# Performance work log

Hardware: AMD Instinct MI355X
Metric: run time of the kernel (lower is better)

Reference implementation:

```python
import jax, jax.numpy as jnp
import numpy as np

EMBED_DIM = 128
B, N = 8, 2048


def entmax15(z):
    """Exact 1.5-entmax along the last axis (Peters & Martins 2019, sort-based)."""
    z = z / 2.0
    z = z - jnp.max(z, axis=-1, keepdims=True)  # shift-invariance -> numerical stability
    zs = -jnp.sort(-z, axis=-1)                 # descending sort
    n = z.shape[-1]
    k = jnp.arange(1, n + 1, dtype=z.dtype)
    mean = jnp.cumsum(zs, axis=-1) / k
    meansq = jnp.cumsum(zs * zs, axis=-1) / k
    ss = k * (meansq - mean * mean)
    delta = (1.0 - ss) / k
    delta_safe = jnp.where(delta > 0, delta, 1.0)
    tau = mean - jnp.where(delta > 0, jnp.sqrt(delta_safe), 0.0)
    support = jnp.sum((tau <= zs).astype(jnp.int32), axis=-1, keepdims=True)
    tau_star = jnp.take_along_axis(tau, support - 1, axis=-1)
    return jnp.square(jnp.maximum(z - tau_star, 0.0))


def setup_inputs() -> dict:
    key = jax.random.key(0)
    ks = jax.random.split(key, 6)
    s = 1.0 / np.sqrt(EMBED_DIM)  # torch nn.Linear default init range
    return {
        "x_c": jax.random.normal(ks[0], (B, N, EMBED_DIM), jnp.float32),
        "x_n": jax.random.normal(ks[1], (B, N, EMBED_DIM), jnp.float32),
        "Wq": jax.random.uniform(ks[2], (EMBED_DIM, EMBED_DIM), jnp.float32, -s, s),
        "bq": jax.random.uniform(ks[3], (EMBED_DIM,), jnp.float32, -s, s),
        "Wk": jax.random.uniform(ks[4], (EMBED_DIM, EMBED_DIM), jnp.float32, -s, s),
        "bk": jax.random.uniform(ks[5], (EMBED_DIM,), jnp.float32, -s, s),
    }


def reference(x_c, x_n, Wq, bq, Wk, bk):
    Q = x_c @ Wq.T + bq                      # [B,N,D]
    K = x_n @ Wk.T + bk                      # [B,N,D]
    A = jnp.einsum("bnd,bmd->bnm", Q, K) / jnp.sqrt(jnp.float32(EMBED_DIM))
    # entmax15 sparse normalization over keys; dropout is identity in eval mode
    return entmax15(A)
```

## Files before the change

kernel.cpp:

```cpp
#include <hip/hip_runtime.h>
#include <hip/hip_bf16.h>

#define BATCH 8
#define SEQ   2048
#define DIM   128
#define NROWS 16384
#define THETA_SPAN 22.62741699796952f

typedef __bf16    bf16x8   __attribute__((ext_vector_type(8)));
typedef float     floatx4  __attribute__((ext_vector_type(4)));
typedef _Float16  half2v   __attribute__((ext_vector_type(2)));

static __device__ __forceinline__ unsigned short f2bf(float v) {
    union { __hip_bfloat16 h; unsigned short u; } c;
    c.h = __float2bfloat16(v);
    return c.u;
}
static __device__ __forceinline__ float bf2f(unsigned short u) {
    union { unsigned int i; float f; } c;
    c.i = (unsigned int)u << 16;
    return c.f;
}
static __device__ __forceinline__ unsigned short f2h(float v) {
    union { _Float16 h; unsigned short u; } c;
    c.h = (_Float16)v;
    return c.u;
}

#if __has_builtin(__builtin_amdgcn_fdot2)
static __device__ __forceinline__ float fdot2acc(half2v a, half2v b, float c) {
    return __builtin_amdgcn_fdot2(a, b, c, false);
}
#else
static __device__ __forceinline__ float fdot2acc(half2v a, half2v b, float c) {
    return fmaf((float)a.y, (float)b.y, fmaf((float)a.x, (float)b.x, c));
}
#endif

__global__ void __launch_bounds__(256)
proj_qk(const float* __restrict__ xq, const float* __restrict__ xn,
        const float* __restrict__ Wq, const float* __restrict__ bq,
        const float* __restrict__ Wk, const float* __restrict__ bk,
        unsigned short* __restrict__ Qhi, unsigned short* __restrict__ Qlo,
        unsigned short* __restrict__ Kb) {
    const int isK = blockIdx.y;
    const float* __restrict__ X    = isK ? xn : xq;
    const float* __restrict__ W    = isK ? Wk : Wq;
    const float* __restrict__ bias = isK ? bk : bq;

    __shared__ float wt[64][133];
    __shared__ float xs[64][68];
    const int tid  = threadIdx.x;
    const int l    = tid & 15;
    const int kthi = tid >> 4;
    const int row0 = blockIdx.x * 64;

    float s[4][8];
#pragma unroll
    for (int rr = 0; rr < 4; ++rr)
#pragma unroll
        for (int j = 0; j < 8; ++j) s[rr][j] = 0.0f;

    for (int ph = 0; ph < 2; ++ph) {
        const int e0 = ph * 64;
#pragma unroll
        for (int i = 0; i < 8; ++i) {
            const int g  = tid + 256 * i;
            const int d  = g >> 4;
            const int c4 = g & 15;
            float4 wv = *reinterpret_cast<const float4*>(
                W + (size_t)d * DIM + e0 + 4 * c4);
            wt[4*c4+0][d] = wv.x;  wt[4*c4+1][d] = wv.y;
            wt[4*c4+2][d] = wv.z;  wt[4*c4+3][d] = wv.w;
        }
#pragma unroll
        for (int i = 0; i < 4; ++i) {
            const int g  = tid + 256 * i;
            const int r  = g >> 4;
            const int c4 = g & 15;
            float4 xv = *reinterpret_cast<const float4*>(
                X + (size_t)(row0 + r) * DIM + e0 + 4 * c4);
            *reinterpret_cast<float4*>(&xs[r][4 * c4]) = xv;
        }
        __syncthreads();
#pragma unroll 8
        for (int e = 0; e < 64; ++e) {
            float w8[8];
            *reinterpret_cast<float4*>(w8)     =
                *reinterpret_cast<const float4*>(&wt[e][kthi * 8]);
            *reinterpret_cast<float4*>(w8 + 4) =
                *reinterpret_cast<const float4*>(&wt[e][kthi * 8 + 4]);
#pragma unroll
            for (int rr = 0; rr < 4; ++rr) {
                const float xv = xs[l + 16 * rr][e];
#pragma unroll
                for (int j = 0; j < 8; ++j) s[rr][j] = fmaf(xv, w8[j], s[rr][j]);
            }
        }
        __syncthreads();
    }

    float b8[8];
    *reinterpret_cast<float4*>(b8)     = *reinterpret_cast<const float4*>(bias + kthi * 8);
    *reinterpret_cast<float4*>(b8 + 4) = *reinterpret_cast<const float4*>(bias + kthi * 8 + 4);

    if (!isK) {
#pragma unroll
        for (int rr = 0; rr < 4; ++rr) {
            const int row = row0 + l + 16 * rr;
            union { uint4 v; unsigned short u[8]; } ph_, pl_;
#pragma unroll
            for (int j = 0; j < 8; ++j) {
                const float v = s[rr][j] + b8[j];
                const unsigned short h = f2bf(v);
                ph_.u[j] = h;
                pl_.u[j] = f2bf(v - bf2f(h));
            }
            const size_t base = ((size_t)kthi * NROWS + row) * 8;
            *reinterpret_cast<uint4*>(Qhi + base) = ph_.v;
            *reinterpret_cast<uint4*>(Qlo + base) = pl_.v;
        }
    } else {
#pragma unroll
        for (int rr = 0; rr < 4; ++rr) {
            const int row = row0 + l + 16 * rr;
            const int b   = row >> 11;
            const int key = row & (SEQ - 1);
            union { uint4 v; unsigned short u[8]; } pk;
#pragma unroll
            for (int j = 0; j < 8; ++j) pk.u[j] = f2bf(s[rr][j] + b8[j]);
            const size_t base = (((size_t)(b * 16) + kthi) * SEQ + key) * 8;
            *reinterpret_cast<uint4*>(Kb + base) = pk.v;
        }
    }
}

__global__ void __launch_bounds__(512, 4)
attn_fused(const __bf16* __restrict__ Qhi, const __bf16* __restrict__ Qlo,
           const __bf16* __restrict__ Kb, float* __restrict__ out) {
    __shared__ unsigned int SW[4 * 4098];
    const int tid  = threadIdx.x;
    const int wv   = tid >> 6;
    const int lane = tid & 63;
    const int l4   = lane & 15;
    const int quad = lane >> 4;
    const int row0 = blockIdx.x * 16;
    const int b    = row0 >> 11;
    const int key0 = wv * 256;

    {
        floatx4 acc[16];
        const floatx4 zerov = {};
#pragma unroll
        for (int t = 0; t < 16; ++t) acc[t] = zerov;

        const size_t qbase = ((size_t)quad * NROWS + row0 + l4) * 8;
        const size_t kbase = (((size_t)(b * 16) + quad) * SEQ + key0 + l4) * 8;
        const size_t qstep = (size_t)4 * NROWS * 8;
        const size_t kstep = (size_t)4 * SEQ * 8;

#pragma unroll
        for (int kt = 0; kt < 4; ++kt) {
            const bf16x8 ah = *reinterpret_cast<const bf16x8*>(Qhi + qbase + kt * qstep);
            const bf16x8 al = *reinterpret_cast<const bf16x8*>(Qlo + qbase + kt * qstep);
            const __bf16* kc = Kb + kbase + kt * kstep;
#pragma unroll
            for (int t = 0; t < 16; ++t) {
                const bf16x8 bkv = *reinterpret_cast<const bf16x8*>(kc + (size_t)t * 128);
                acc[t] = __builtin_amdgcn_mfma_f32_16x16x32_bf16(ah, bkv, acc[t], 0, 0, 0);
                acc[t] = __builtin_amdgcn_mfma_f32_16x16x32_bf16(al, bkv, acc[t], 0, 0, 0);
            }
        }
#pragma unroll
        for (int t = 0; t < 16; ++t) {
            union { uint2 v; unsigned short u[4]; } pk;
#pragma unroll
            for (int bb = 0; bb < 4; ++bb) pk.u[bb] = f2h(acc[t][bb]);
            const int key = key0 + t * 16 + l4;
            *reinterpret_cast<uint2*>(&SW[quad * 4098 + 2 * key]) = pk.v;
        }
    }
    __syncthreads();

    const int g  = wv >> 1;
    const int sp = wv & 1;

    const unsigned int* Sw = &SW[g * 4098];
    unsigned int raw[32];
#pragma unroll
    for (int c = 0; c < 32; ++c) raw[c] = Sw[2 * (c * 64 + lane) + sp];

    half2v z0[16], z1[16];
#pragma unroll
    for (int i = 0; i < 16; ++i) {
        union { unsigned int u; half2v h; } c0, c1;
        c0.u = __builtin_amdgcn_perm(raw[2 * i + 1], raw[2 * i], 0x05040100u);
        c1.u = __builtin_amdgcn_perm(raw[2 * i + 1], raw[2 * i], 0x07060302u);
        z0[i] = c0.h;
        z1[i] = c1.h;
    }

    const half2v hzero = {(_Float16)0.0f, (_Float16)0.0f};

    float m0 = -1e30f, m1 = -1e30f;
#pragma unroll
    for (int i = 0; i < 16; ++i) {
        m0 = fmaxf(m0, fmaxf((float)z0[i].x, (float)z0[i].y));
        m1 = fmaxf(m1, fmaxf((float)z1[i].x, (float)z1[i].y));
    }
#pragma unroll
    for (int off = 32; off >= 1; off >>= 1) {
        m0 = fmaxf(m0, __shfl_xor(m0, off, 64));
        m1 = fmaxf(m1, __shfl_xor(m1, off, 64));
    }

    float lo0 = m0 - THETA_SPAN, hi0 = m0;
    float lo1 = m1 - THETA_SPAN, hi1 = m1;
    for (int it = 0; it < 11; ++it) {
        const float th0 = 0.5f * (lo0 + hi0);
        const float th1 = 0.5f * (lo1 + hi1);
        const _Float16 t0h = (_Float16)th0;
        const _Float16 t1h = (_Float16)th1;
        const half2v n0 = {(_Float16)-t0h, (_Float16)-t0h};
        const half2v n1 = {(_Float16)-t1h, (_Float16)-t1h};
        float f0 = 0.0f, f1 = 0.0f;
#pragma unroll
        for (int i = 0; i < 16; ++i) {
            half2v d0 = z0[i] + n0;
            half2v d1 = z1[i] + n1;
            d0 = __builtin_elementwise_max(d0, hzero);
            d1 = __builtin_elementwise_max(d1, hzero);
            f0 = fdot2acc(d0, d0, f0);
            f1 = fdot2acc(d1, d1, f1);
        }
#pragma unroll
        for (int off = 32; off >= 1; off >>= 1) {
            f0 += __shfl_xor(f0, off, 64);
            f1 += __shfl_xor(f1, off, 64);
        }
        if (f0 >= 512.0f) lo0 = th0; else hi0 = th0;
        if (f1 >= 512.0f) lo1 = th1; else hi1 = th1;
    }
    float th0 = 0.5f * (lo0 + hi0);
    float th1 = 0.5f * (lo1 + hi1);
    th0 = (float)((_Float16)th0);
    th1 = (float)((_Float16)th1);

    float* o0 = out + (size_t)(row0 + 4 * g + 2 * sp + 0) * SEQ + lane;
    float* o1 = out + (size_t)(row0 + 4 * g + 2 * sp + 1) * SEQ + lane;
#pragma unroll
    for (int i = 0; i < 16; ++i) {
        const float a0 = fmaxf((float)z0[i].x - th0, 0.0f);
        const float a1 = fmaxf((float)z0[i].y - th0, 0.0f);
        const float b0 = fmaxf((float)z1[i].x - th1, 0.0f);
        const float b1 = fmaxf((float)z1[i].y - th1, 0.0f);
        o0[(size_t)(2 * i) * 64]     = a0 * a0 * (1.0f / 512.0f);
        o0[(size_t)(2 * i + 1) * 64] = a1 * a1 * (1.0f / 512.0f);
        o1[(size_t)(2 * i) * 64]     = b0 * b0 * (1.0f / 512.0f);
        o1[(size_t)(2 * i + 1) * 64] = b1 * b1 * (1.0f / 512.0f);
    }
}

extern "C" void kernel_launch(void* const* d_in, const int* in_sizes, int n_in,
                              void* d_out, int out_size, void* d_ws, size_t ws_size,
                              hipStream_t stream) {
    const float* x_c = (const float*)d_in[0];
    const float* x_n = (const float*)d_in[1];
    const float* Wq  = (const float*)d_in[2];
    const float* bq  = (const float*)d_in[3];
    const float* Wk  = (const float*)d_in[4];
    const float* bk  = (const float*)d_in[5];
    float* out = (float*)d_out;

    char* ws = (char*)d_ws;
    unsigned short* Qhi = (unsigned short*)ws;
    unsigned short* Qlo = (unsigned short*)(ws + ((size_t)4 << 20));
    unsigned short* Kbl = (unsigned short*)(ws + ((size_t)8 << 20));

    proj_qk<<<dim3(NROWS / 64, 2), 256, 0, stream>>>(
        x_c, x_n, Wq, bq, Wk, bk, Qhi, Qlo, Kbl);
    attn_fused<<<NROWS / 16, 512, 0, stream>>>(
        (const __bf16*)Qhi, (const __bf16*)Qlo, (const __bf16*)Kbl, out);
}
```

Measured before the change: 200.7 us.

## Compute Q/K projections with bf16 MFMA using split-precision inputs

Replaces the scalar FP32 FMA projection with MFMA 16x16x32 bf16 instructions. X is split into hi/lo bf16 parts and W is rounded to bf16. Results are staged in shared memory and then written out in the same packed layouts. This moves the small projection GEMM onto matrix cores. W now uses a single bf16 term, so the projection loses some precision, which could shift entmax support near the threshold.

Result: faster. 193.6 us (-3.5%).

```diff
diff --git a/kernel.cpp b/kernel.cpp
--- a/kernel.cpp
+++ b/kernel.cpp
@@ -37,7 +37,7 @@
 }
 #endif
 
-__global__ void __launch_bounds__(256)
+__global__ void __launch_bounds__(256, 2)
 proj_qk(const float* __restrict__ xq, const float* __restrict__ xn,
         const float* __restrict__ Wq, const float* __restrict__ bq,
         const float* __restrict__ Wk, const float* __restrict__ bk,
@@ -48,89 +48,114 @@
     const float* __restrict__ W    = isK ? Wk : Wq;
     const float* __restrict__ bias = isK ? bk : bq;
 
-    __shared__ float wt[64][133];
-    __shared__ float xs[64][68];
+    __shared__ __align__(16) unsigned short SM[34816];
+    unsigned short* XH = SM;
+    unsigned short* XL = SM + 8704;
+    unsigned short* WW = SM + 17408;
+
     const int tid  = threadIdx.x;
+    const int lane = tid & 63;
+    const int wv   = tid >> 6;
+    const int l4   = lane & 15;
+    const int quad = lane >> 4;
+    const int row0 = blockIdx.x * 64;
+
+#pragma unroll
+    for (int i = 0; i < 8; ++i) {
+        const int g  = tid + 256 * i;
+        const int r  = g >> 5;
+        const int c4 = g & 31;
+        const float4 xv = *reinterpret_cast<const float4*>(
+            X + (size_t)(row0 + r) * DIM + 4 * c4);
+        union { ushort2 v[2]; unsigned short u[4]; } hh, ll;
+        const float xf[4] = {xv.x, xv.y, xv.z, xv.w};
+#pragma unroll
+        for (int j = 0; j < 4; ++j) {
+            const unsigned short h = f2bf(xf[j]);
+            hh.u[j] = h;
+            ll.u[j] = f2bf(xf[j] - bf2f(h));
+        }
+        *reinterpret_cast<uint2*>(&XH[r * 136 + 4 * c4]) =
+            *reinterpret_cast<uint2*>(hh.u);
+        *reinterpret_cast<uint2*>(&XL[r * 136 + 4 * c4]) =
+            *reinterpret_cast<uint2*>(ll.u);
+    }
+#pragma unroll
+    for (int i = 0; i < 16; ++i) {
+        const int g  = tid + 256 * i;
+        const int d  = g >> 5;
+        const int c4 = g & 31;
+        const float4 wvv = *reinterpret_cast<const float4*>(
+            W + (size_t)d * DIM + 4 * c4);
+        union { uint2 v; unsigned short u[4]; } pw;
+        pw.u[0] = f2bf(wvv.x); pw.u[1] = f2bf(wvv.y);
+        pw.u[2] = f2bf(wvv.z); pw.u[3] = f2bf(wvv.w);
+        *reinterpret_cast<uint2*>(&WW[d * 136 + 4 * c4]) = pw.v;
+    }
+    __syncthreads();
+
+    floatx4 acc[8];
+    const floatx4 zerov = {};
+#pragma unroll
+    for (int mt = 0; mt < 8; ++mt) acc[mt] = zerov;
+
+#pragma unroll
+    for (int kt = 0; kt < 4; ++kt) {
+        const int koff = kt * 32 + quad * 8;
+        const bf16x8 xh = *reinterpret_cast<const bf16x8*>(
+            &XH[(wv * 16 + l4) * 136 + koff]);
+        const bf16x8 xl = *reinterpret_cast<const bf16x8*>(
+            &XL[(wv * 16 + l4) * 136 + koff]);
+#pragma unroll
+        for (int mt = 0; mt < 8; ++mt) {
+            const bf16x8 wf = *reinterpret_cast<const bf16x8*>(
+                &WW[(mt * 16 + l4) * 136 + koff]);
+            acc[mt] = __builtin_amdgcn_mfma_f32_16x16x32_bf16(wf, xh, acc[mt], 0, 0, 0);
+            acc[mt] = __builtin_amdgcn_mfma_f32_16x16x32_bf16(wf, xl, acc[mt], 0, 0, 0);
+        }
+    }
+
+    const int erow = wv * 16 + l4;
+#pragma unroll
+    for (int mt = 0; mt < 8; ++mt) {
+        const float4 bv = *reinterpret_cast<const float4*>(bias + mt * 16 + quad * 4);
+        const float bf[4] = {bv.x, bv.y, bv.z, bv.w};
+        union { uint2 v; unsigned short u[4]; } hh, ll;
+#pragma unroll
+        for (int r = 0; r < 4; ++r) {
+            const float v = acc[mt][r] + bf[r];
+            const unsigned short h = f2bf(v);
+            hh.u[r] = h;
+            ll.u[r] = f2bf(v - bf2f(h));
+        }
+        const int off = erow * 136 + mt * 16 + quad * 4;
+        *reinterpret_cast<uint2*>(&XH[off]) = hh.v;
+        if (!isK) *reinterpret_cast<uint2*>(&XL[off]) = ll.v;
+    }
+    __syncthreads();
+
     const int l    = tid & 15;
     const int kthi = tid >> 4;
-    const int row0 = blockIdx.x * 64;
-
-    float s[4][8];
-#pragma unroll
-    for (int rr = 0; rr < 4; ++rr)
-#pragma unroll
-        for (int j = 0; j < 8; ++j) s[rr][j] = 0.0f;
-
-    for (int ph = 0; ph < 2; ++ph) {
-        const int e0 = ph * 64;
-#pragma unroll
-        for (int i = 0; i < 8; ++i) {
-            const int g  = tid + 256 * i;
-            const int d  = g >> 4;
-            const int c4 = g & 15;
-            float4 wv = *reinterpret_cast<const float4*>(
-                W + (size_t)d * DIM + e0 + 4 * c4);
-            wt[4*c4+0][d] = wv.x;  wt[4*c4+1][d] = wv.y;
-            wt[4*c4+2][d] = wv.z;  wt[4*c4+3][d] = wv.w;
-        }
-#pragma unroll
-        for (int i = 0; i < 4; ++i) {
-            const int g  = tid + 256 * i;
-            const int r  = g >> 4;
-            const int c4 = g & 15;
-            float4 xv = *reinterpret_cast<const float4*>(
-                X + (size_t)(row0 + r) * DIM + e0 + 4 * c4);
-            *reinterpret_cast<float4*>(&xs[r][4 * c4]) = xv;
-        }
-        __syncthreads();
-#pragma unroll 8
-        for (int e = 0; e < 64; ++e) {
-            float w8[8];
-            *reinterpret_cast<float4*>(w8)     =
-                *reinterpret_cast<const float4*>(&wt[e][kthi * 8]);
-            *reinterpret_cast<float4*>(w8 + 4) =
-                *reinterpret_cast<const float4*>(&wt[e][kthi * 8 + 4]);
-#pragma unroll
-            for (int rr = 0; rr < 4; ++rr) {
-                const float xv = xs[l + 16 * rr][e];
-#pragma unroll
-                for (int j = 0; j < 8; ++j) s[rr][j] = fmaf(xv, w8[j], s[rr][j]);
-            }
-        }
-        __syncthreads();
-    }
-
-    float b8[8];
-    *reinterpret_cast<float4*>(b8)     = *reinterpret_cast<const float4*>(bias + kthi * 8);
-    *reinterpret_cast<float4*>(b8 + 4) = *reinterpret_cast<const float4*>(bias + kthi * 8 + 4);
-
     if (!isK) {
 #pragma unroll
         for (int rr = 0; rr < 4; ++rr) {
-            const int row = row0 + l + 16 * rr;
-            union { uint4 v; unsigned short u[8]; } ph_, pl_;
-#pragma unroll
-            for (int j = 0; j < 8; ++j) {
-                const float v = s[rr][j] + b8[j];
-                const unsigned short h = f2bf(v);
-                ph_.u[j] = h;
-                pl_.u[j] = f2bf(v - bf2f(h));
-            }
-            const size_t base = ((size_t)kthi * NROWS + row) * 8;
-            *reinterpret_cast<uint4*>(Qhi + base) = ph_.v;
-            *reinterpret_cast<uint4*>(Qlo + base) = pl_.v;
+            const int row = l + 16 * rr;
+            const uint4 ph = *reinterpret_cast<const uint4*>(&XH[row * 136 + kthi * 8]);
+            const uint4 pl = *reinterpret_cast<const uint4*>(&XL[row * 136 + kthi * 8]);
+            const size_t base = ((size_t)kthi * NROWS + row0 + row) * 8;
+            *reinterpret_cast<uint4*>(Qhi + base) = ph;
+            *reinterpret_cast<uint4*>(Qlo + base) = pl;
         }
     } else {
 #pragma unroll
         for (int rr = 0; rr < 4; ++rr) {
-            const int row = row0 + l + 16 * rr;
-            const int b   = row >> 11;
-            const int key = row & (SEQ - 1);
-            union { uint4 v; unsigned short u[8]; } pk;
-#pragma unroll
-            for (int j = 0; j < 8; ++j) pk.u[j] = f2bf(s[rr][j] + b8[j]);
+            const int row = l + 16 * rr;
+            const int grow = row0 + row;
+            const int b    = grow >> 11;
+            const int key  = grow & (SEQ - 1);
+            const uint4 pk = *reinterpret_cast<const uint4*>(&XH[row * 136 + kthi * 8]);
             const size_t base = (((size_t)(b * 16) + kthi) * SEQ + key) * 8;
-            *reinterpret_cast<uint4*>(Kb + base) = pk.v;
+            *reinterpret_cast<uint4*>(Kb + base) = pk;
         }
     }
 }
```
